# Kernel tuning notes

Hardware: AMD Instinct MI355X
Metric: run time of the kernel (lower is better)

## Reference

```python
import jax, jax.numpy as jnp
import numpy as np

B, C, H, W = 2, 512, 64, 64
GROUPS = 32
EPS = 1e-6


def setup_inputs() -> dict:
    key = jax.random.key(0)
    ks = jax.random.split(key, 9)
    s = 1.0 / np.sqrt(C)
    return {
        "x": jax.random.normal(ks[0], (B, C, H, W), dtype=jnp.float32),
        "gamma": jnp.ones((C,), dtype=jnp.float32),
        "beta": jnp.zeros((C,), dtype=jnp.float32),
        "wq": jax.random.normal(ks[1], (C, C), dtype=jnp.float32) * s,
        "bq": jnp.zeros((C,), dtype=jnp.float32),
        "wk": jax.random.normal(ks[2], (C, C), dtype=jnp.float32) * s,
        "bk": jnp.zeros((C,), dtype=jnp.float32),
        "wv": jax.random.normal(ks[3], (C, C), dtype=jnp.float32) * s,
        "bv": jnp.zeros((C,), dtype=jnp.float32),
        "wp": jax.random.normal(ks[4], (C, C), dtype=jnp.float32) * s,
        "bp": jnp.zeros((C,), dtype=jnp.float32),
    }


def _group_norm(x, gamma, beta):
    b, c, h, w = x.shape
    xg = x.reshape(b, GROUPS, c // GROUPS, h, w)
    mean = jnp.mean(xg, axis=(2, 3, 4), keepdims=True)
    var = jnp.var(xg, axis=(2, 3, 4), keepdims=True)
    xn = ((xg - mean) * jax.lax.rsqrt(var + EPS)).reshape(b, c, h, w)
    return xn * gamma[None, :, None, None] + beta[None, :, None, None]


def reference(x, gamma, beta, wq, bq, wk, bk, wv, bv, wp, bp):
    b, c, h, w = x.shape
    hn = _group_norm(x, gamma, beta)
    # 1x1 convs == per-pixel linear; flatten spatial: (b, hw, c)
    t = hn.reshape(b, c, h * w).transpose(0, 2, 1)
    q = jnp.einsum('bnc,oc->bno', t, wq) + bq
    k = jnp.einsum('bnc,oc->bno', t, wk) + bk
    v = jnp.einsum('bnc,oc->bno', t, wv) + bv
    scale = float(int(c) ** (-0.5))
    attn = jax.nn.softmax(jnp.einsum('bic,bjc->bij', q, k) * scale, axis=-1)
    o = jnp.einsum('bij,bjc->bic', attn, v)  # (b, hw, c)
    o = jnp.einsum('bnc,oc->bno', o, wp) + bp
    o = o.transpose(0, 2, 1).reshape(b, c, h, w)
    return x + o
```

## Files before the change

### kernel.cpp

```cpp
#include <hip/hip_runtime.h>
#include <hip/hip_bf16.h>

#define B_ 2
#define C_ 512
#define HW_ 4096
#define K_ 512
#define EPS_ 1e-6f
#define SCALE_ 0.04419417382415922f
#define NEG_INF_ (-1e30f)

typedef __attribute__((ext_vector_type(8))) __bf16 bf16x8;
typedef __attribute__((ext_vector_type(4))) float f32x4;
typedef __attribute__((ext_vector_type(16))) float f32x16;

__device__ __forceinline__ unsigned short f2bf(float f) {
  union { float f; unsigned u; } v; v.f = f;
  unsigned r = v.u + 0x7fffu + ((v.u >> 16) & 1u);
  return (unsigned short)(r >> 16);
}
__device__ __forceinline__ float bf2f(unsigned short h) {
  union { unsigned u; float f; } v; v.u = ((unsigned)h) << 16;
  return v.f;
}

__device__ __forceinline__ void gld_lds16(const unsigned short* g, unsigned short* l) {
  __builtin_amdgcn_global_load_lds((const __attribute__((address_space(1))) void*)g,
                                   (__attribute__((address_space(3))) void*)l, 16, 0, 0);
}

__global__ void gn_cast(const float* __restrict__ x, float* __restrict__ pstats,
                        const float* __restrict__ s0, const float* __restrict__ s1,
                        const float* __restrict__ s2, const float* __restrict__ s3,
                        unsigned short* __restrict__ dst) {
  int bid = blockIdx.x;
  int t = threadIdx.x;
  if (bid < 1024) {
    int bg = bid >> 4, row = bid & 15;
    int b = bg >> 5, g = bg & 31;
    const float* base = x + ((size_t)(b * C_ + g * 16 + row)) * HW_;
    float s = 0.f, s2 = 0.f;
    #pragma unroll
    for (int i = 0; i < 4; ++i) {
      float4 v = *reinterpret_cast<const float4*>(base + (size_t)(t + i * 256) * 4);
      s  += v.x + v.y + v.z + v.w;
      s2 += v.x * v.x + v.y * v.y + v.z * v.z + v.w * v.w;
    }
    for (int off = 32; off; off >>= 1) { s += __shfl_down(s, off); s2 += __shfl_down(s2, off); }
    __shared__ float rs[4], rs2[4];
    int w = t >> 6;
    if ((t & 63) == 0) { rs[w] = s; rs2[w] = s2; }
    __syncthreads();
    if (t == 0) {
      pstats[bid] = rs[0] + rs[1] + rs[2] + rs[3];
      pstats[1024 + bid] = rs2[0] + rs2[1] + rs2[2] + rs2[3];
    }
  } else {
    int cid = bid - 1024;
    int which = cid >> 8, bx = cid & 255;
    const float* src = which == 0 ? s0 : which == 1 ? s1 : which == 2 ? s2 : s3;
    int i = (bx * 256 + t) * 4;
    float4 v = *reinterpret_cast<const float4*>(src + i);
    ushort4 o; o.x = f2bf(v.x); o.y = f2bf(v.y); o.z = f2bf(v.z); o.w = f2bf(v.w);
    *reinterpret_cast<ushort4*>(dst + (size_t)which * 262144 + i) = o;
  }
}

__global__ void build_t(const float* __restrict__ x, const float* __restrict__ pstats,
                        const float* __restrict__ gamma, const float* __restrict__ beta,
                        unsigned short* __restrict__ tb) {
  __shared__ float lds[64 * 69];
  int n0 = blockIdx.x * 64, c0 = blockIdx.y * 64, b = blockIdx.z;
  int t = threadIdx.x;
  {
    int cl = t >> 2, ch = t & 3;
    int c = c0 + cl;
    int bg = b * 32 + (c >> 4);
    float s = 0.f, s2v = 0.f;
    #pragma unroll
    for (int r = 0; r < 16; ++r) {
      s   += pstats[bg * 16 + r];
      s2v += pstats[1024 + bg * 16 + r];
    }
    float mean = s * (1.f / 65536.f);
    float var = s2v * (1.f / 65536.f) - mean * mean;
    float rstd = rsqrtf(var + EPS_);
    float ga = gamma[c] * rstd;
    float be = beta[c] - mean * ga;
    const float* xr = x + ((size_t)(b * C_ + c)) * HW_ + n0 + ch * 16;
    #pragma unroll
    for (int i = 0; i < 4; ++i) {
      float4 v = *reinterpret_cast<const float4*>(xr + i * 4);
      int nl = ch * 16 + i * 4;
      lds[cl * 69 + nl + 0] = v.x * ga + be;
      lds[cl * 69 + nl + 1] = v.y * ga + be;
      lds[cl * 69 + nl + 2] = v.z * ga + be;
      lds[cl * 69 + nl + 3] = v.w * ga + be;
    }
  }
  __syncthreads();
  {
    int nl = t >> 2, cw = t & 3;
    unsigned short* orow = tb + ((size_t)(b * HW_ + n0 + nl)) * C_ + c0 + cw * 16;
    #pragma unroll
    for (int i = 0; i < 4; ++i) {
      ushort4 o4;
      o4.x = f2bf(lds[(cw * 16 + i * 4 + 0) * 69 + nl]);
      o4.y = f2bf(lds[(cw * 16 + i * 4 + 1) * 69 + nl]);
      o4.z = f2bf(lds[(cw * 16 + i * 4 + 2) * 69 + nl]);
      o4.w = f2bf(lds[(cw * 16 + i * 4 + 3) * 69 + nl]);
      *reinterpret_cast<ushort4*>(orow + i * 4) = o4;
    }
  }
}

__global__ __launch_bounds__(256, 2) void gemm_qkv(
    const unsigned short* __restrict__ tb, const unsigned short* __restrict__ wqkv,
    const float* __restrict__ bq, const float* __restrict__ bk, const float* __restrict__ bv,
    unsigned short* __restrict__ qb, unsigned short* __restrict__ kb,
    unsigned short* __restrict__ vTb) {
  __shared__ unsigned short Al[2][128 * 64];
  __shared__ unsigned short Bl[2][128 * 64];
  int f = blockIdx.x + 4 * (blockIdx.y + 32 * blockIdx.z);
  int xcd = f & 7, i = f >> 3;
  int bx = i & 3;
  int g = xcd * 24 + (i >> 2);
  int bz = g >> 5, by = g & 31;
  int which = bz >> 1, b = bz & 1;
  const unsigned short* Ab = (which < 2) ? (tb + (size_t)b * HW_ * K_) : (wqkv + 2 * 262144);
  const unsigned short* Bb = (which < 2) ? (wqkv + which * 262144) : (tb + (size_t)b * HW_ * K_);
  int m0 = (which < 2) ? by * 128 : bx * 128;
  int n0 = (which < 2) ? bx * 128 : by * 128;
  int N = (which < 2) ? 512 : HW_;
  unsigned short* Cb = (which == 0) ? (qb + (size_t)b * HW_ * K_)
                     : (which == 1) ? (kb + (size_t)b * HW_ * K_)
                                    : (vTb + (size_t)b * C_ * HW_);
  const float* bias = (which == 0) ? bq : (which == 1) ? bk : bv;
  int t = threadIdx.x, lane = t & 63, w = t >> 6;
  int l15 = lane & 15, quad = lane >> 4;
  int mw = (w & 1) * 64, nw = (w >> 1) * 64;
  int sr8 = lane >> 3, sb = lane & 7;
  f32x4 acc[4][4] = {};

  #define G_STAGE(KC) do {                                                          \
    int pb = (KC) & 1;                                                              \
    _Pragma("unroll")                                                               \
    for (int q = 0; q < 4; ++q) {                                                   \
      int row = w * 32 + q * 8 + sr8;                                               \
      int gb = sb ^ (row & 7);                                                      \
      gld_lds16(Ab + (size_t)(m0 + row) * K_ + (KC) * 64 + gb * 8, &Al[pb][(w * 32 + q * 8) * 64]); \
      gld_lds16(Bb + (size_t)(n0 + row) * K_ + (KC) * 64 + gb * 8, &Bl[pb][(w * 32 + q * 8) * 64]); \
    }                                                                               \
  } while (0)

  G_STAGE(0);
  __syncthreads();
  for (int kc = 0; kc < 8; ++kc) {
    if (kc < 7) G_STAGE(kc + 1);
    const unsigned short* Ac = Al[kc & 1];
    const unsigned short* Bc = Bl[kc & 1];
    #pragma unroll
    for (int kk = 0; kk < 2; ++kk) {
      bf16x8 af[4];
      #pragma unroll
      for (int mt = 0; mt < 4; ++mt)
        af[mt] = *reinterpret_cast<const bf16x8*>(
            &Ac[(mw + mt * 16 + l15) * 64 + (((kk * 4 + quad) ^ (l15 & 7)) << 3)]);
      #pragma unroll
      for (int nt = 0; nt < 4; ++nt) {
        bf16x8 bfr = *reinterpret_cast<const bf16x8*>(
            &Bc[(nw + nt * 16 + l15) * 64 + (((kk * 4 + quad) ^ (l15 & 7)) << 3)]);
        #pragma unroll
        for (int mt = 0; mt < 4; ++mt)
          acc[mt][nt] = __builtin_amdgcn_mfma_f32_16x16x32_bf16(af[mt], bfr, acc[mt][nt], 0, 0, 0);
      }
    }
    __syncthreads();
  }
  #undef G_STAGE
  #pragma unroll
  for (int mt = 0; mt < 4; ++mt)
    #pragma unroll
    for (int nt = 0; nt < 4; ++nt)
      #pragma unroll
      for (int rr = 0; rr < 4; ++rr) {
        int row = m0 + mw + mt * 16 + quad * 4 + rr;
        int col = n0 + nw + nt * 16 + l15;
        float v = acc[mt][nt][rr] + ((which < 2) ? bias[col] : bias[row]);
        Cb[(size_t)row * N + col] = f2bf(v);
      }
}

__global__ __launch_bounds__(256, 2) void gemm_fin(
    const unsigned short* __restrict__ A,
    const unsigned short* __restrict__ opart,
    const float* __restrict__ mpart, const float* __restrict__ lpart,
    const float* __restrict__ bias, const float* __restrict__ resid,
    float* __restrict__ out) {
  __shared__ unsigned short Al[2][128 * 64];
  __shared__ unsigned short Bl[2][64 * 68];
  int z = blockIdx.z;
  int n0 = blockIdx.x * 64, m0 = blockIdx.y * 128;
  int t = threadIdx.x, lane = t & 63, w = t >> 6;
  int l15 = lane & 15, quad = lane >> 4;
  int mw = (w & 1) * 64, nw = (w >> 1) * 32;
  int sr8 = lane >> 3, sb = lane & 7;
  f32x4 acc[4][2] = {};

  float w0[2], w1[2];
  int nrow[2];
  #pragma unroll
  for (int q = 0; q < 2; ++q) {
    int n = n0 + w * 16 + q * 8 + sr8;
    nrow[q] = n;
    float ma = mpart[(size_t)z * HW_ + n], mb = mpart[(size_t)(2 + z) * HW_ + n];
    float la = lpart[(size_t)z * HW_ + n], lb = lpart[(size_t)(2 + z) * HW_ + n];
    float M = fmaxf(ma, mb);
    float ea = __expf(ma - M), eb = __expf(mb - M);
    float iv = 1.f / (la * ea + lb * eb);
    w0[q] = ea * iv; w1[q] = eb * iv;
  }
  const unsigned short* p0 = opart + (size_t)z * HW_ * 512;
  const unsigned short* p1 = opart + (size_t)(2 + z) * HW_ * 512;

  #define STAGE_A(KC) do {                                                          \
    int pb = (KC) & 1;                                                              \
    _Pragma("unroll")                                                               \
    for (int q = 0; q < 4; ++q) {                                                   \
      int row = w * 32 + q * 8 + sr8;                                               \
      int gb = sb ^ (row & 7);                                                      \
      gld_lds16(A + (size_t)(m0 + row) * K_ + (KC) * 64 + gb * 8, &Al[pb][(w * 32 + q * 8) * 64]); \
    }                                                                               \
  } while (0)

  #define STAGE_B(KC) do {                                                          \
    int pb = (KC) & 1;                                                              \
    _Pragma("unroll")                                                               \
    for (int q = 0; q < 2; ++q) {                                                   \
      int row = w * 16 + q * 8 + sr8;                                               \
      size_t goff = (size_t)nrow[q] * 512 + (KC) * 64 + sb * 8;                     \
      uint4 u0 = *reinterpret_cast<const uint4*>(p0 + goff);                        \
      uint4 u1 = *reinterpret_cast<const uint4*>(p1 + goff);                        \
      uint4 o4;                                                                     \
      unsigned* a0 = reinterpret_cast<unsigned*>(&u0);                              \
      unsigned* a1 = reinterpret_cast<unsigned*>(&u1);                              \
      unsigned* od = reinterpret_cast<unsigned*>(&o4);                              \
      _Pragma("unroll")                                                             \
      for (int j = 0; j < 4; ++j) {                                                 \
        float lo = bf2f((unsigned short)(a0[j] & 0xffffu)) * w0[q]                  \
                 + bf2f((unsigned short)(a1[j] & 0xffffu)) * w1[q];                 \
        float hi = bf2f((unsigned short)(a0[j] >> 16)) * w0[q]                      \
                 + bf2f((unsigned short)(a1[j] >> 16)) * w1[q];                     \
        od[j] = (unsigned)f2bf(lo) | ((unsigned)f2bf(hi) << 16);                    \
      }                                                                             \
      *reinterpret_cast<uint4*>(&Bl[pb][row * 68 + sb * 8]) = o4;                   \
    }                                                                               \
  } while (0)

  STAGE_A(0);
  STAGE_B(0);
  __syncthreads();
  for (int kc = 0; kc < 8; ++kc) {
    if (kc < 7) { STAGE_A(kc + 1); STAGE_B(kc + 1); }
    const unsigned short* Ac = Al[kc & 1];
    const unsigned short* Bc = Bl[kc & 1];
    #pragma unroll
    for (int kk = 0; kk < 2; ++kk) {
      bf16x8 af[4];
      #pragma unroll
      for (int mt = 0; mt < 4; ++mt)
        af[mt] = *reinterpret_cast<const bf16x8*>(
            &Ac[(mw + mt * 16 + l15) * 64 + (((kk * 4 + quad) ^ (l15 & 7)) << 3)]);
      #pragma unroll
      for (int nt = 0; nt < 2; ++nt) {
        bf16x8 bfr = *reinterpret_cast<const bf16x8*>(
            &Bc[(nw + nt * 16 + l15) * 68 + ((kk * 4 + quad) << 3)]);
        #pragma unroll
        for (int mt = 0; mt < 4; ++mt)
          acc[mt][nt] = __builtin_amdgcn_mfma_f32_16x16x32_bf16(af[mt], bfr, acc[mt][nt], 0, 0, 0);
      }
    }
    __syncthreads();
  }
  #undef STAGE_A
  #undef STAGE_B
  #pragma unroll
  for (int mt = 0; mt < 4; ++mt)
    #pragma unroll
    for (int nt = 0; nt < 2; ++nt)
      #pragma unroll
      for (int rr = 0; rr < 4; ++rr) {
        int row = m0 + mw + mt * 16 + quad * 4 + rr;
        int col = n0 + nw + nt * 16 + l15;
        size_t idx = (size_t)z * (C_ * HW_) + (size_t)row * HW_ + col;
        out[idx] = acc[mt][nt][rr] + bias[row] + resid[idx];
      }
}

__global__ __launch_bounds__(512, 2) void attn(
    const unsigned short* __restrict__ qg, const unsigned short* __restrict__ kg,
    const unsigned short* __restrict__ vg,
    unsigned short* __restrict__ opart, float* __restrict__ mpart, float* __restrict__ lpart) {
  __shared__ unsigned short KVb[4 * 16384];
  __shared__ unsigned short Pl[64 * 136];
  __shared__ float sm_m[64], sm_l[64], sm_alpha[64], sm_red[128];
  int qt = blockIdx.x, jh = blockIdx.y, b = blockIdx.z;
  int t = threadIdx.x, lane = t & 63, w = t >> 6;
  int l15 = lane & 15, quad = lane >> 4;
  int l31 = lane & 31, hl = lane >> 5;
  int rw = w & 3, cw = w >> 2;
  int rw2 = w & 1, dg = w >> 1;
  int m0 = qt * 64;
  if (t < 64) { sm_m[t] = NEG_INF_; sm_l[t] = 0.f; }

  int st_r[4], st_kb[4];
  #pragma unroll
  for (int q = 0; q < 4; ++q) {
    int blk = w * 4 + q;
    st_r[q] = blk * 4 + (lane >> 4);
    st_kb[q] = (lane & 15) ^ (st_r[q] & 7);
  }

  #define STAGE_K(JC, KC, J0, BUF) do {                                             \
    const unsigned short* gb = kg + ((size_t)(b * HW_ + (J0) + (JC) * 128)) * K_ + (KC) * 128; \
    unsigned short* lb = KVb + ((BUF) << 14);                                       \
    _Pragma("unroll")                                                               \
    for (int q = 0; q < 4; ++q)                                                     \
      gld_lds16(gb + (size_t)st_r[q] * K_ + st_kb[q] * 8, lb + (w * 4 + q) * 512);  \
  } while (0)

  #define STAGE_V(DC, JC, J0, BUF) do {                                             \
    const unsigned short* gb = vg + ((size_t)(b * K_ + (DC) * 128)) * HW_ + (J0) + (JC) * 128; \
    unsigned short* lb = KVb + ((BUF) << 14);                                       \
    _Pragma("unroll")                                                               \
    for (int q = 0; q < 4; ++q)                                                     \
      gld_lds16(gb + (size_t)st_r[q] * HW_ + st_kb[q] * 8, lb + (w * 4 + q) * 512); \
  } while (0)

  bf16x8 qa[16];
  {
    const unsigned short* qrow = qg + ((size_t)(b * HW_ + m0 + rw * 16 + l15)) * K_ + quad * 8;
    #pragma unroll
    for (int kk = 0; kk < 16; ++kk)
      qa[kk] = *reinterpret_cast<const bf16x8*>(qrow + kk * 32);
  }
  f32x16 acc_o[4] = {};

  int j0 = jh * 2048;
  STAGE_K(0, 0, j0, 0);
  STAGE_K(0, 1, j0, 1);
  __syncthreads();

  for (int it = 0; it < 8; ++it, j0 += 256) {
    f32x4 acc_s[8] = {};
    #pragma unroll
    for (int c = 0; c < 8; ++c) {
      if ((c & 1) == 0) {
        if (c < 6) {
          STAGE_K((c + 2) >> 2, (c + 2) & 3, j0, (c + 2) & 3);
          STAGE_K((c + 3) >> 2, (c + 3) & 3, j0, (c + 3) & 3);
        } else {
          STAGE_V(0, 0, j0, 0);
          STAGE_V(1, 0, j0, 1);
        }
      }
      const unsigned short* bufc = KVb + ((c & 3) << 14);
      int jc = c >> 2, kc = c & 3;
      __builtin_amdgcn_s_setprio(1);
      #pragma unroll
      for (int kk = 0; kk < 4; ++kk)
        #pragma unroll
        for (int ct = 0; ct < 4; ++ct) {
          int jr = cw * 64 + ct * 16 + l15;
          bf16x8 bfr = *reinterpret_cast<const bf16x8*>(
              &bufc[jr * 128 + (((kk * 4 + quad) ^ (l15 & 7)) << 3)]);
          acc_s[jc * 4 + ct] = __builtin_amdgcn_mfma_f32_16x16x32_bf16(qa[kc * 4 + kk], bfr, acc_s[jc * 4 + ct], 0, 0, 0);
        }
      __builtin_amdgcn_s_setprio(0);
      if (c & 1) __syncthreads();
    }
    float mx[4];
    #pragma unroll
    for (int rr = 0; rr < 4; ++rr) {
      float m = NEG_INF_;
      #pragma unroll
      for (int s = 0; s < 8; ++s) {
        acc_s[s][rr] *= SCALE_;
        m = fmaxf(m, acc_s[s][rr]);
      }
      mx[rr] = m;
    }
    #pragma unroll
    for (int off = 1; off < 16; off <<= 1)
      #pragma unroll
      for (int rr = 0; rr < 4; ++rr)
        mx[rr] = fmaxf(mx[rr], __shfl_xor(mx[rr], off));
    if (l15 == 0)
      #pragma unroll
      for (int rr = 0; rr < 4; ++rr)
        sm_red[cw * 64 + rw * 16 + quad * 4 + rr] = mx[rr];
    __syncthreads();
    if (t < 64) {
      float mnew = fmaxf(sm_m[t], fmaxf(sm_red[t], sm_red[64 + t]));
      sm_alpha[t] = __expf(sm_m[t] - mnew);
      sm_m[t] = mnew;
    }
    __syncthreads();
    float sum[4] = {0.f, 0.f, 0.f, 0.f};
    #pragma unroll
    for (int s = 0; s < 8; ++s)
      #pragma unroll
      for (int rr = 0; rr < 4; ++rr) {
        int rowl = rw * 16 + quad * 4 + rr;
        float p = __expf(acc_s[s][rr] - sm_m[rowl]);
        sum[rr] += p;
        if (s < 4)
          Pl[rowl * 136 + cw * 64 + (s & 3) * 16 + l15] = f2bf(p);
      }
    #pragma unroll
    for (int off = 1; off < 16; off <<= 1)
      #pragma unroll
      for (int rr = 0; rr < 4; ++rr)
        sum[rr] += __shfl_xor(sum[rr], off);
    if (l15 == 0)
      #pragma unroll
      for (int rr = 0; rr < 4; ++rr)
        sm_red[cw * 64 + rw * 16 + quad * 4 + rr] = sum[rr];
    __syncthreads();
    if (t < 64)
      sm_l[t] = sm_l[t] * sm_alpha[t] + sm_red[t] + sm_red[64 + t];
    #pragma unroll
    for (int r16 = 0; r16 < 16; ++r16) {
      int row = rw2 * 32 + (r16 & 3) + 8 * (r16 >> 2) + 4 * hl;
      float a = sm_alpha[row];
      #pragma unroll
      for (int dc = 0; dc < 4; ++dc)
        acc_o[dc][r16] *= a;
    }
    bf16x8 pa_r[8];
    #pragma unroll
    for (int c = 0; c < 8; ++c) {
      if (c == 2) {
        #pragma unroll
        for (int s = 4; s < 8; ++s)
          #pragma unroll
          for (int rr = 0; rr < 4; ++rr) {
            int rowl = rw * 16 + quad * 4 + rr;
            Pl[rowl * 136 + cw * 64 + (s & 3) * 16 + l15] =
                f2bf(__expf(acc_s[s][rr] - sm_m[rowl]));
          }
      }
      if ((c & 3) == 0) {
        #pragma unroll
        for (int ksx = 0; ksx < 8; ++ksx)
          pa_r[ksx] = *reinterpret_cast<const bf16x8*>(
              &Pl[(rw2 * 32 + l31) * 136 + ksx * 16 + hl * 8]);
      }
      if ((c & 1) == 0) {
        if (c < 6) {
          STAGE_V((c + 2) & 3, (c + 2) >> 2, j0, (c + 2) & 3);
          STAGE_V((c + 3) & 3, (c + 3) >> 2, j0, (c + 3) & 3);
        } else if (it < 7) {
          STAGE_K(0, 0, j0 + 256, 0);
          STAGE_K(0, 1, j0 + 256, 1);
        }
      }
      const unsigned short* bufc = KVb + ((c & 3) << 14);
      int dc = c & 3;
      __builtin_amdgcn_s_setprio(1);
      #pragma unroll
      for (int ksx = 0; ksx < 8; ++ksx) {
        bf16x8 vb = *reinterpret_cast<const bf16x8*>(
            &bufc[(dg * 32 + l31) * 128 + (((ksx * 2 + hl) ^ (l31 & 7)) << 3)]);
        acc_o[dc] = __builtin_amdgcn_mfma_f32_32x32x16_bf16(pa_r[ksx], vb, acc_o[dc], 0, 0, 0);
      }
      __builtin_amdgcn_s_setprio(0);
      if (c & 1) __syncthreads();
    }
  }
  #undef STAGE_K
  #undef STAGE_V
  int part = jh * 2 + b;
  unsigned short* ob = opart + ((size_t)part * HW_ + m0) * 512;
  #pragma unroll
  for (int dc = 0; dc < 4; ++dc) {
    int d = dc * 128 + dg * 32 + l31;
    #pragma unroll
    for (int r16 = 0; r16 < 16; ++r16) {
      int row = rw2 * 32 + (r16 & 3) + 8 * (r16 >> 2) + 4 * hl;
      ob[(size_t)row * 512 + d] = f2bf(acc_o[dc][r16]);
    }
  }
  if (t < 64) {
    mpart[(size_t)part * HW_ + m0 + t] = sm_m[t];
    lpart[(size_t)part * HW_ + m0 + t] = sm_l[t];
  }
}

extern "C" void kernel_launch(void* const* d_in, const int* in_sizes, int n_in,
                              void* d_out, int out_size, void* d_ws, size_t ws_size,
                              hipStream_t stream) {
  const float* x     = (const float*)d_in[0];
  const float* gamma = (const float*)d_in[1];
  const float* beta  = (const float*)d_in[2];
  const float* wq    = (const float*)d_in[3];
  const float* bq    = (const float*)d_in[4];
  const float* wk    = (const float*)d_in[5];
  const float* bk    = (const float*)d_in[6];
  const float* wv    = (const float*)d_in[7];
  const float* bv    = (const float*)d_in[8];
  const float* wp    = (const float*)d_in[9];
  const float* bp    = (const float*)d_in[10];
  float* out = (float*)d_out;

  char* ws = (char*)d_ws;
  size_t o = 0;
  float* pstats         = (float*)(ws + o);          o += 8192;
  unsigned short* tb    = (unsigned short*)(ws + o); o += 8388608;
  unsigned short* qb    = (unsigned short*)(ws + o); o += 8388608;
  unsigned short* kb    = (unsigned short*)(ws + o); o += 8388608;
  unsigned short* vTb   = (unsigned short*)(ws + o); o += 8388608;
  unsigned short* wqb   = (unsigned short*)(ws + o); o += 524288;
  unsigned short* wkb   = (unsigned short*)(ws + o); o += 524288;
  unsigned short* wvb   = (unsigned short*)(ws + o); o += 524288;
  unsigned short* wpb   = (unsigned short*)(ws + o); o += 524288;
  unsigned short* opart = (unsigned short*)(ws + o); o += 16777216;
  float* mpart          = (float*)(ws + o);          o += 65536;
  float* lpart          = (float*)(ws + o);          o += 65536;

  gn_cast<<<2048, 256, 0, stream>>>(x, pstats, wq, wk, wv, wp, wqb);
  build_t<<<dim3(64, 8, 2), 256, 0, stream>>>(x, pstats, gamma, beta, tb);
  gemm_qkv<<<dim3(4, 32, 6), 256, 0, stream>>>(tb, wqb, bq, bk, bv, qb, kb, vTb);
  attn<<<dim3(64, 2, 2), 512, 0, stream>>>(qb, kb, vTb, opart, mpart, lpart);
  gemm_fin<<<dim3(64, 4, 2), 256, 0, stream>>>(wpb, opart, mpart, lpart, bp, x, out);
}
```

Baseline: 249.5 us.

## Fold group-norm affine into QKV weights and bias to avoid second pass over x

The group-norm scale and shift are folded into per-batch QKV weights (W*gamma*rstd) and biases (b + W*beta'). x is then read only once, in a kernel that both accumulates partial group statistics and transposes the raw x to bf16. A small weight-prep kernel reduces the statistics and writes per-batch scaled bf16 weights. This removes one full read of x, but the GEMM now runs on un-normalized bf16 activations, which can cost precision when group means are large.

Measured after the change: 262.1 us. 1.05x slower.

```diff
diff --git a/kernel.cpp b/kernel.cpp
--- a/kernel.cpp
+++ b/kernel.cpp
@@ -28,76 +28,39 @@
                                    (__attribute__((address_space(3))) void*)l, 16, 0, 0);
 }
 
-__global__ void gn_cast(const float* __restrict__ x, float* __restrict__ pstats,
-                        const float* __restrict__ s0, const float* __restrict__ s1,
-                        const float* __restrict__ s2, const float* __restrict__ s3,
-                        unsigned short* __restrict__ dst) {
-  int bid = blockIdx.x;
-  int t = threadIdx.x;
-  if (bid < 1024) {
-    int bg = bid >> 4, row = bid & 15;
-    int b = bg >> 5, g = bg & 31;
-    const float* base = x + ((size_t)(b * C_ + g * 16 + row)) * HW_;
-    float s = 0.f, s2 = 0.f;
-    #pragma unroll
-    for (int i = 0; i < 4; ++i) {
-      float4 v = *reinterpret_cast<const float4*>(base + (size_t)(t + i * 256) * 4);
-      s  += v.x + v.y + v.z + v.w;
-      s2 += v.x * v.x + v.y * v.y + v.z * v.z + v.w * v.w;
-    }
-    for (int off = 32; off; off >>= 1) { s += __shfl_down(s, off); s2 += __shfl_down(s2, off); }
-    __shared__ float rs[4], rs2[4];
-    int w = t >> 6;
-    if ((t & 63) == 0) { rs[w] = s; rs2[w] = s2; }
-    __syncthreads();
-    if (t == 0) {
-      pstats[bid] = rs[0] + rs[1] + rs[2] + rs[3];
-      pstats[1024 + bid] = rs2[0] + rs2[1] + rs2[2] + rs2[3];
-    }
-  } else {
-    int cid = bid - 1024;
-    int which = cid >> 8, bx = cid & 255;
-    const float* src = which == 0 ? s0 : which == 1 ? s1 : which == 2 ? s2 : s3;
-    int i = (bx * 256 + t) * 4;
-    float4 v = *reinterpret_cast<const float4*>(src + i);
-    ushort4 o; o.x = f2bf(v.x); o.y = f2bf(v.y); o.z = f2bf(v.z); o.w = f2bf(v.w);
-    *reinterpret_cast<ushort4*>(dst + (size_t)which * 262144 + i) = o;
-  }
-}
-
-__global__ void build_t(const float* __restrict__ x, const float* __restrict__ pstats,
-                        const float* __restrict__ gamma, const float* __restrict__ beta,
-                        unsigned short* __restrict__ tb) {
+__global__ void sum_t(const float* __restrict__ x, float* __restrict__ pstats,
+                      unsigned short* __restrict__ tb) {
   __shared__ float lds[64 * 69];
+  __shared__ float ps[64], ps2[64];
   int n0 = blockIdx.x * 64, c0 = blockIdx.y * 64, b = blockIdx.z;
   int t = threadIdx.x;
   {
     int cl = t >> 2, ch = t & 3;
-    int c = c0 + cl;
-    int bg = b * 32 + (c >> 4);
-    float s = 0.f, s2v = 0.f;
-    #pragma unroll
-    for (int r = 0; r < 16; ++r) {
-      s   += pstats[bg * 16 + r];
-      s2v += pstats[1024 + bg * 16 + r];
-    }
-    float mean = s * (1.f / 65536.f);
-    float var = s2v * (1.f / 65536.f) - mean * mean;
-    float rstd = rsqrtf(var + EPS_);
-    float ga = gamma[c] * rstd;
-    float be = beta[c] - mean * ga;
-    const float* xr = x + ((size_t)(b * C_ + c)) * HW_ + n0 + ch * 16;
+    const float* xr = x + ((size_t)(b * C_ + c0 + cl)) * HW_ + n0 + ch * 16;
+    float s = 0.f, s2 = 0.f;
     #pragma unroll
     for (int i = 0; i < 4; ++i) {
       float4 v = *reinterpret_cast<const float4*>(xr + i * 4);
       int nl = ch * 16 + i * 4;
-      lds[cl * 69 + nl + 0] = v.x * ga + be;
-      lds[cl * 69 + nl + 1] = v.y * ga + be;
-      lds[cl * 69 + nl + 2] = v.z * ga + be;
-      lds[cl * 69 + nl + 3] = v.w * ga + be;
-    }
+      lds[cl * 69 + nl + 0] = v.x;
+      lds[cl * 69 + nl + 1] = v.y;
+      lds[cl * 69 + nl + 2] = v.z;
+      lds[cl * 69 + nl + 3] = v.w;
+      s  += v.x + v.y + v.z + v.w;
+      s2 += v.x * v.x + v.y * v.y + v.z * v.z + v.w * v.w;
+    }
+    s += __shfl_xor(s, 1); s2 += __shfl_xor(s2, 1);
+    s += __shfl_xor(s, 2); s2 += __shfl_xor(s2, 2);
+    if (ch == 0) { ps[cl] = s; ps2[cl] = s2; }
   }
   __syncthreads();
+  if (t < 4) {
+    float a = 0.f, a2 = 0.f;
+    #pragma unroll
+    for (int k = 0; k < 16; ++k) { a += ps[t * 16 + k]; a2 += ps2[t * 16 + k]; }
+    int idx = ((b * 8 + blockIdx.y) * 4 + t) * 64 + blockIdx.x;
+    pstats[idx] = a; pstats[4096 + idx] = a2;
+  }
   {
     int nl = t >> 2, cw = t & 3;
     unsigned short* orow = tb + ((size_t)(b * HW_ + n0 + nl)) * C_ + c0 + cw * 16;
@@ -113,9 +76,70 @@
   }
 }
 
+__global__ void wprep(const float* __restrict__ pstats,
+                      const float* __restrict__ gamma, const float* __restrict__ beta,
+                      const float* __restrict__ wq, const float* __restrict__ wk,
+                      const float* __restrict__ wv, const float* __restrict__ wp,
+                      const float* __restrict__ bq, const float* __restrict__ bk,
+                      const float* __restrict__ bv,
+                      unsigned short* __restrict__ wqkvb, float* __restrict__ biasb) {
+  int which = blockIdx.y, b = blockIdx.z;
+  if (which == 3 && b == 1) return;
+  int t = threadIdx.x;
+  __shared__ float sg[32], sg2[32], ga[512], be[512];
+  if (which < 3) {
+    if (t < 64) {
+      int g = t & 31, hf = t >> 5;
+      const float* base = pstats + hf * 4096 + (size_t)(b * 32 + g) * 64;
+      float a = 0.f;
+      for (int k = 0; k < 64; ++k) a += base[k];
+      if (hf) sg2[g] = a; else sg[g] = a;
+    }
+    __syncthreads();
+    for (int c = t; c < 512; c += 256) {
+      int g = c >> 4;
+      float mean = sg[g] * (1.f / 65536.f);
+      float var = sg2[g] * (1.f / 65536.f) - mean * mean;
+      float rstd = rsqrtf(var + EPS_);
+      float gav = gamma[c] * rstd;
+      ga[c] = gav; be[c] = beta[c] - mean * gav;
+    }
+    __syncthreads();
+  }
+  const float* w = which == 0 ? wq : which == 1 ? wk : which == 2 ? wv : wp;
+  int ol = t >> 2, ch = t & 3;
+  int o = blockIdx.x * 64 + ol;
+  const float* wr = w + (size_t)o * 512 + ch * 128;
+  unsigned short* wo = wqkvb + (size_t)(which < 3 ? (which * 2 + b) : 6) * 262144
+                     + (size_t)o * 512 + ch * 128;
+  float pd = 0.f;
+  #pragma unroll 8
+  for (int i = 0; i < 32; ++i) {
+    float4 v = *reinterpret_cast<const float4*>(wr + i * 4);
+    int c = ch * 128 + i * 4;
+    ushort4 o4;
+    if (which < 3) {
+      pd += be[c] * v.x + be[c + 1] * v.y + be[c + 2] * v.z + be[c + 3] * v.w;
+      o4.x = f2bf(v.x * ga[c]);     o4.y = f2bf(v.y * ga[c + 1]);
+      o4.z = f2bf(v.z * ga[c + 2]); o4.w = f2bf(v.w * ga[c + 3]);
+    } else {
+      o4.x = f2bf(v.x); o4.y = f2bf(v.y); o4.z = f2bf(v.z); o4.w = f2bf(v.w);
+    }
+    *reinterpret_cast<ushort4*>(wo + i * 4) = o4;
+  }
+  if (which < 3) {
+    pd += __shfl_xor(pd, 1);
+    pd += __shfl_xor(pd, 2);
+    if (ch == 0) {
+      const float* b0 = which == 0 ? bq : which == 1 ? bk : bv;
+      biasb[(which * 2 + b) * 512 + o] = b0[o] + pd;
+    }
+  }
+}
+
 __global__ __launch_bounds__(256, 2) void gemm_qkv(
-    const unsigned short* __restrict__ tb, const unsigned short* __restrict__ wqkv,
-    const float* __restrict__ bq, const float* __restrict__ bk, const float* __restrict__ bv,
+    const unsigned short* __restrict__ tb, const unsigned short* __restrict__ wqkvb,
+    const float* __restrict__ biasb,
     unsigned short* __restrict__ qb, unsigned short* __restrict__ kb,
     unsigned short* __restrict__ vTb) {
   __shared__ unsigned short Al[2][128 * 64];
@@ -126,15 +150,17 @@
   int g = xcd * 24 + (i >> 2);
   int bz = g >> 5, by = g & 31;
   int which = bz >> 1, b = bz & 1;
-  const unsigned short* Ab = (which < 2) ? (tb + (size_t)b * HW_ * K_) : (wqkv + 2 * 262144);
-  const unsigned short* Bb = (which < 2) ? (wqkv + which * 262144) : (tb + (size_t)b * HW_ * K_);
+  const unsigned short* Ab = (which < 2) ? (tb + (size_t)b * HW_ * K_)
+                                         : (wqkvb + (size_t)(4 + b) * 262144);
+  const unsigned short* Bb = (which < 2) ? (wqkvb + (size_t)(which * 2 + b) * 262144)
+                                         : (tb + (size_t)b * HW_ * K_);
   int m0 = (which < 2) ? by * 128 : bx * 128;
   int n0 = (which < 2) ? bx * 128 : by * 128;
   int N = (which < 2) ? 512 : HW_;
   unsigned short* Cb = (which == 0) ? (qb + (size_t)b * HW_ * K_)
                      : (which == 1) ? (kb + (size_t)b * HW_ * K_)
                                     : (vTb + (size_t)b * C_ * HW_);
-  const float* bias = (which == 0) ? bq : (which == 1) ? bk : bv;
+  const float* bias = biasb + (which * 2 + b) * 512;
   int t = threadIdx.x, lane = t & 63, w = t >> 6;
   int l15 = lane & 15, quad = lane >> 4;
   int mw = (w & 1) * 64, nw = (w >> 1) * 64;
@@ -514,22 +540,22 @@
 
   char* ws = (char*)d_ws;
   size_t o = 0;
-  float* pstats         = (float*)(ws + o);          o += 8192;
+  float* pstats         = (float*)(ws + o);          o += 32768;
+  float* biasb          = (float*)(ws + o);          o += 16384;
   unsigned short* tb    = (unsigned short*)(ws + o); o += 8388608;
   unsigned short* qb    = (unsigned short*)(ws + o); o += 8388608;
   unsigned short* kb    = (unsigned short*)(ws + o); o += 8388608;
   unsigned short* vTb   = (unsigned short*)(ws + o); o += 8388608;
-  unsigned short* wqb   = (unsigned short*)(ws + o); o += 524288;
-  unsigned short* wkb   = (unsigned short*)(ws + o); o += 524288;
-  unsigned short* wvb   = (unsigned short*)(ws + o); o += 524288;
-  unsigned short* wpb   = (unsigned short*)(ws + o); o += 524288;
+  unsigned short* wqkvb = (unsigned short*)(ws + o); o += 4194304;
   unsigned short* opart = (unsigned short*)(ws + o); o += 16777216;
   float* mpart          = (float*)(ws + o);          o += 65536;
   float* lpart          = (float*)(ws + o);          o += 65536;
 
-  gn_cast<<<2048, 256, 0, stream>>>(x, pstats, wq, wk, wv, wp, wqb);
-  build_t<<<dim3(64, 8, 2), 256, 0, stream>>>(x, pstats, gamma, beta, tb);
-  gemm_qkv<<<dim3(4, 32, 6), 256, 0, stream>>>(tb, wqb, bq, bk, bv, qb, kb, vTb);
+  sum_t<<<dim3(64, 8, 2), 256, 0, stream>>>(x, pstats, tb);
+  wprep<<<dim3(8, 4, 2), 256, 0, stream>>>(pstats, gamma, beta, wq, wk, wv, wp,
+                                           bq, bk, bv, wqkvb, biasb);
+  gemm_qkv<<<dim3(4, 32, 6), 256, 0, stream>>>(tb, wqkvb, biasb, qb, kb, vTb);
   attn<<<dim3(64, 2, 2), 512, 0, stream>>>(qb, kb, vTb, opart, mpart, lpart);
-  gemm_fin<<<dim3(64, 4, 2), 256, 0, stream>>>(wpb, opart, mpart, lpart, bp, x, out);
-}
+  gemm_fin<<<dim3(64, 4, 2), 256, 0, stream>>>(wqkvb + (size_t)6 * 262144, opart,
+                                               mpart, lpart, bp, x, out);
+}
```
